# Performance work log

Hardware: AMD Instinct MI355X
Metric: run time of the kernel (lower is better)

Reference implementation:

```python
import jax, jax.numpy as jnp
import numpy as np

K = 3            # receptive_field
N = 50000        # num_nodes
E = 800000       # num_edges
D = 128          # feature dim


def setup_inputs() -> dict:
    key = jax.random.key(0)
    k1, k2, k3 = jax.random.split(key, 3)
    x = jax.random.normal(k1, (N, D), dtype=jnp.float32)
    edge_index = jax.random.randint(k2, (2, E), 0, N, dtype=jnp.int64)
    edge_weight = jax.random.uniform(k3, (E,), dtype=jnp.float32)
    return {"x": x, "edge_index": edge_index, "edge_weight": edge_weight}


def _gcn_norm(edge_weight, row, col, num_nodes):
    # symmetric GCN normalization: w_ij / sqrt(deg_i * deg_j), in-degree at target
    deg = jax.ops.segment_sum(edge_weight, col, num_segments=num_nodes)
    dinv = jnp.where(deg > 0, jax.lax.rsqrt(deg), 0.0)
    return dinv[row] * edge_weight * dinv[col]


def _propagate(x, row, col, w, num_nodes):
    # out[i] = sum_{(j->i) in E} w_ji * x[j]   (gather-scale-scatter)
    msgs = x[row] * w[:, None]                 # [E, D]
    return jax.ops.segment_sum(msgs, col, num_segments=num_nodes)


def reference(x, edge_index, edge_weight):
    num_nodes = x.shape[-2]
    row, col = edge_index[0], edge_index[1]
    w = _gcn_norm(edge_weight, row, col, num_nodes)
    out = [x]
    xk = x
    for _ in range(K):
        xk = _propagate(xk, row, col, w, num_nodes)
        out.append(xk)
    # global attribute: broadcast node-mean to every node
    g = jnp.broadcast_to(jnp.mean(x, axis=-2, keepdims=True), x.shape)
    out.append(g)
    return jnp.concatenate(out, axis=-1)   # [N, (K+2)*D]
```

## Files before the change

kernel.cpp:

```cpp
#include <hip/hip_runtime.h>


#define D 128
#define OUTC4 160
#define CAP 64
#define CH 8
#define PB 256
#define CB 512
#define BCAP 5120

__device__ inline unsigned short f2bf(float f) {
    unsigned u = __float_as_uint(f);
    u += 0x7FFFu + ((u >> 16) & 1u);
    return (unsigned short)(u >> 16);
}
__device__ inline float bfhi(unsigned u) {
    return __uint_as_float(u & 0xFFFF0000u);
}
__device__ inline float bflo(unsigned u) {
    return __uint_as_float(u << 16);
}
__device__ inline unsigned pack2(float lo, float hi) {
    return ((unsigned)f2bf(hi) << 16) | (unsigned)f2bf(lo);
}
__device__ inline void fma8(float4& a0, float4& a1, float w, uint4 v) {
    a0.x += w * bflo(v.x); a0.y += w * bfhi(v.x);
    a0.z += w * bflo(v.y); a0.w += w * bfhi(v.y);
    a1.x += w * bflo(v.z); a1.y += w * bfhi(v.z);
    a1.z += w * bflo(v.w); a1.w += w * bfhi(v.w);
}

__global__ void k_part(const int* __restrict__ row, const int* __restrict__ col,
                       const float* __restrict__ ew, const float* __restrict__ x,
                       int* __restrict__ bcur, uint2* __restrict__ breg,
                       float* __restrict__ gsum, int E, int N) {
    __shared__ int shi[512];
    if ((int)blockIdx.x < PB) {
        int* hist = shi;
        int* base = shi + 256;
        int rng = (E + PB - 1) / PB;
        int e0 = blockIdx.x * rng;
        int e1 = e0 + rng; if (e1 > E) e1 = E;
        hist[threadIdx.x] = 0;
        __syncthreads();
        for (int e = e0 + (int)threadIdx.x; e < e1; e += 256)
            atomicAdd(&hist[(unsigned)col[e] >> 8], 1);
        __syncthreads();
        int h = hist[threadIdx.x];
        if (h) base[threadIdx.x] = atomicAdd(&bcur[threadIdx.x], h);
        __syncthreads();
        hist[threadIdx.x] = 0;
        __syncthreads();
        for (int e = e0 + (int)threadIdx.x; e < e1; e += 256) {
            int c = col[e];
            int b = (unsigned)c >> 8;
            int r = atomicAdd(&hist[b], 1);
            int pos = base[b] + r;
            if (pos < BCAP)
                breg[(size_t)b * BCAP + pos] =
                    make_uint2(((unsigned)f2bf(ew[e]) << 16) | (unsigned)row[e], (unsigned)c);
        }
    } else {
        float* sh = (float*)shi;
        int bid = blockIdx.x - PB;
        int f = threadIdx.x & 127;
        int sub = threadIdx.x >> 7;
        float acc = 0.f;
        for (int n = bid * 2 + sub; n < N; n += CB * 2)
            acc += x[(size_t)n * D + f];
        if (sub) sh[f] = acc;
        __syncthreads();
        if (!sub) atomicAdd(&gsum[f], acc + sh[f]);
    }
}

__global__ void k_prep(const int* __restrict__ bcur, const uint2* __restrict__ breg,
                       int* __restrict__ cnt, float* __restrict__ dinv,
                       unsigned* __restrict__ slots, const float4* __restrict__ x4,
                       const float* __restrict__ gsum, float4* __restrict__ out4,
                       uint4* __restrict__ xb0, int N, int GB, float invN) {
    __shared__ int shi[512];
    if ((int)blockIdx.x < GB) {
        int* ncur = shi;
        float* wsum = (float*)(shi + 256);
        int b = blockIdx.x;
        ncur[threadIdx.x] = 0;
        wsum[threadIdx.x] = 0.f;
        __syncthreads();
        int cb = bcur[b]; if (cb > BCAP) cb = BCAP;
        const uint2* br = breg + (size_t)b * BCAP;
        for (int i = threadIdx.x; i < cb; i += 256) {
            uint2 ed = br[i];
            int node = (int)ed.y;
            int l = node & 255;
            int r = atomicAdd(&ncur[l], 1);
            if (r < CAP) slots[(size_t)node * CAP + r] = ed.x;
            atomicAdd(&wsum[l], bfhi(ed.x));
        }
        __syncthreads();
        int node = b * 256 + (int)threadIdx.x;
        if (node < N) {
            cnt[node] = ncur[threadIdx.x];
            float v = wsum[threadIdx.x];
            dinv[node] = v > 0.f ? rsqrtf(v) : 0.f;
        }
    } else {
        int t = (blockIdx.x - GB) * 256 + threadIdx.x;
        if (t >= N * 16) return;
        int n = t >> 4;
        int q = t & 15;
        float4 v0 = x4[(size_t)n * 32 + 2 * q];
        float4 v1 = x4[(size_t)n * 32 + 2 * q + 1];
        size_t ob = (size_t)n * OUTC4;
        out4[ob + 2 * q] = v0;
        out4[ob + 2 * q + 1] = v1;
        xb0[(size_t)n * 16 + q] = make_uint4(pack2(v0.x, v0.y), pack2(v0.z, v0.w),
                                             pack2(v1.x, v1.y), pack2(v1.z, v1.w));
        int g = 8 * q;
        out4[ob + 128 + 2 * q] = make_float4(gsum[g] * invN, gsum[g + 1] * invN,
                                             gsum[g + 2] * invN, gsum[g + 3] * invN);
        out4[ob + 129 + 2 * q] = make_float4(gsum[g + 4] * invN, gsum[g + 5] * invN,
                                             gsum[g + 6] * invN, gsum[g + 7] * invN);
    }
}

template <bool NORM>
__global__ void k_prop(const int* __restrict__ cnt, unsigned* __restrict__ slots,
                       const float* __restrict__ dinv, const uint4* __restrict__ xin,
                       float4* __restrict__ out4, uint4* __restrict__ xout,
                       int N, int out_off4, int writeb) {
    int t = blockIdx.x * blockDim.x + threadIdx.x;
    int node = t >> 4;
    if (node >= N) return;
    int lane = t & 15;
    int c = cnt[node]; if (c > CAP) c = CAP;
    unsigned* s = slots + (size_t)node * CAP;
    float dd = NORM ? dinv[node] : 0.f;
    float4 a0 = make_float4(0.f, 0.f, 0.f, 0.f);
    float4 a1 = make_float4(0.f, 0.f, 0.f, 0.f);
    int i = 0;
    for (; i + CH <= c; i += CH) {
        unsigned sl[CH]; float w[CH]; uint4 v[CH];
#pragma unroll
        for (int j = 0; j < CH; j++) sl[j] = s[i + j];
#pragma unroll
        for (int j = 0; j < CH; j++)
            w[j] = NORM ? dd * bfhi(sl[j]) * dinv[sl[j] & 0xFFFFu] : bfhi(sl[j]);
        if (NORM && lane == 0) {
#pragma unroll
            for (int j = 0; j < CH; j++)
                s[i + j] = ((unsigned)f2bf(w[j]) << 16) | (sl[j] & 0xFFFFu);
        }
#pragma unroll
        for (int j = 0; j < CH; j++) v[j] = xin[(size_t)(sl[j] & 0xFFFFu) * 16 + lane];
#pragma unroll
        for (int j = 0; j < CH; j++) fma8(a0, a1, w[j], v[j]);
    }
    if (i < c) {
        unsigned sl[CH]; float w[CH]; uint4 v[CH];
#pragma unroll
        for (int j = 0; j < CH; j++) {
            int idx = (i + j < c) ? i + j : c - 1;
            sl[j] = s[idx];
        }
#pragma unroll
        for (int j = 0; j < CH; j++) {
            float ww = NORM ? dd * bfhi(sl[j]) * dinv[sl[j] & 0xFFFFu] : bfhi(sl[j]);
            w[j] = (i + j < c) ? ww : 0.f;
        }
        if (NORM && lane == 0) {
#pragma unroll
            for (int j = 0; j < CH; j++)
                if (i + j < c) s[i + j] = ((unsigned)f2bf(w[j]) << 16) | (sl[j] & 0xFFFFu);
        }
#pragma unroll
        for (int j = 0; j < CH; j++) v[j] = xin[(size_t)(sl[j] & 0xFFFFu) * 16 + lane];
#pragma unroll
        for (int j = 0; j < CH; j++) fma8(a0, a1, w[j], v[j]);
    }
    size_t ob = (size_t)node * OUTC4 + out_off4 + 2 * lane;
    out4[ob] = a0;
    out4[ob + 1] = a1;
    if (writeb)
        xout[(size_t)node * 16 + lane] =
            make_uint4(pack2(a0.x, a0.y), pack2(a0.z, a0.w),
                       pack2(a1.x, a1.y), pack2(a1.z, a1.w));
}

extern "C" void kernel_launch(void* const* d_in, const int* in_sizes, int n_in,
                              void* d_out, int out_size, void* d_ws, size_t ws_size,
                              hipStream_t stream) {
    const float* x = (const float*)d_in[0];
    const int* ei = (const int*)d_in[1];
    const float* ew = (const float*)d_in[2];
    float* out = (float*)d_out;

    int N = in_sizes[0] / D;
    int E = in_sizes[2];
    const int* row = ei;
    const int* colp = ei + E;

    int* bcur = (int*)d_ws;
    float* gsum = (float*)(bcur + 256);
    int* cnt = (int*)(gsum + 128);
    float* dinv = (float*)(cnt + N);
    unsigned* slots = (unsigned*)(dinv + N);
    uint2* breg = (uint2*)(slots + (size_t)N * CAP);
    uint4* xb0 = (uint4*)(breg + (size_t)PB * BCAP);
    uint4* xb1 = xb0 + (size_t)N * 16;

    hipMemsetAsync(d_ws, 0, 384 * sizeof(int), stream);

    k_part<<<PB + CB, 256, 0, stream>>>(row, colp, ew, x, bcur, breg, gsum, E, N);

    int GB = (N + 255) / 256;
    int IB = (N * 16 + 255) / 256;
    k_prep<<<GB + IB, 256, 0, stream>>>(bcur, breg, cnt, dinv, slots, (const float4*)x,
                                        gsum, (float4*)out, xb0, N, GB, 1.f / (float)N);

    int pblocks = (N * 16 + 255) / 256;
    k_prop<true><<<pblocks, 256, 0, stream>>>(cnt, slots, dinv, xb0, (float4*)out, xb1, N, 32, 1);
    k_prop<false><<<pblocks, 256, 0, stream>>>(cnt, slots, dinv, xb1, (float4*)out, xb0, N, 64, 1);
    k_prop<false><<<pblocks, 256, 0, stream>>>(cnt, slots, dinv, xb0, (float4*)out, xb1, N, 96, 0);
}
```

Baseline: 283.2 us.

## Split later propagation hops into feature-slice passes and use nontemporal stores

```diff
diff --git a/kernel.cpp b/kernel.cpp
--- a/kernel.cpp
+++ b/kernel.cpp
@@ -8,6 +8,18 @@
 #define PB 256
 #define CB 512
 #define BCAP 5120
+
+typedef float f4v __attribute__((ext_vector_type(4)));
+typedef unsigned u4v __attribute__((ext_vector_type(4)));
+
+__device__ inline void nt_store_f4(float4* p, float4 v) {
+    f4v t = {v.x, v.y, v.z, v.w};
+    __builtin_nontemporal_store(t, (f4v*)p);
+}
+__device__ inline void nt_store_u4(uint4* p, uint4 v) {
+    u4v t = {v.x, v.y, v.z, v.w};
+    __builtin_nontemporal_store(t, (u4v*)p);
+}
 
 __device__ inline unsigned short f2bf(float f) {
     unsigned u = __float_as_uint(f);
@@ -112,30 +124,32 @@
         float4 v0 = x4[(size_t)n * 32 + 2 * q];
         float4 v1 = x4[(size_t)n * 32 + 2 * q + 1];
         size_t ob = (size_t)n * OUTC4;
-        out4[ob + 2 * q] = v0;
-        out4[ob + 2 * q + 1] = v1;
-        xb0[(size_t)n * 16 + q] = make_uint4(pack2(v0.x, v0.y), pack2(v0.z, v0.w),
-                                             pack2(v1.x, v1.y), pack2(v1.z, v1.w));
+        nt_store_f4(&out4[ob + 2 * q], v0);
+        nt_store_f4(&out4[ob + 2 * q + 1], v1);
+        nt_store_u4(&xb0[(size_t)n * 16 + q],
+                    make_uint4(pack2(v0.x, v0.y), pack2(v0.z, v0.w),
+                               pack2(v1.x, v1.y), pack2(v1.z, v1.w)));
         int g = 8 * q;
-        out4[ob + 128 + 2 * q] = make_float4(gsum[g] * invN, gsum[g + 1] * invN,
-                                             gsum[g + 2] * invN, gsum[g + 3] * invN);
-        out4[ob + 129 + 2 * q] = make_float4(gsum[g + 4] * invN, gsum[g + 5] * invN,
-                                             gsum[g + 6] * invN, gsum[g + 7] * invN);
-    }
-}
-
-template <bool NORM>
-__global__ void k_prop(const int* __restrict__ cnt, unsigned* __restrict__ slots,
-                       const float* __restrict__ dinv, const uint4* __restrict__ xin,
-                       float4* __restrict__ out4, uint4* __restrict__ xout,
-                       int N, int out_off4, int writeb) {
+        nt_store_f4(&out4[ob + 128 + 2 * q],
+                    make_float4(gsum[g] * invN, gsum[g + 1] * invN,
+                                gsum[g + 2] * invN, gsum[g + 3] * invN));
+        nt_store_f4(&out4[ob + 129 + 2 * q],
+                    make_float4(gsum[g + 4] * invN, gsum[g + 5] * invN,
+                                gsum[g + 6] * invN, gsum[g + 7] * invN));
+    }
+}
+
+__global__ void k_prop1(const int* __restrict__ cnt, unsigned* __restrict__ slots,
+                        const float* __restrict__ dinv, const uint4* __restrict__ xin,
+                        float4* __restrict__ out4, uint4* __restrict__ xout,
+                        int N, int out_off4) {
     int t = blockIdx.x * blockDim.x + threadIdx.x;
     int node = t >> 4;
     if (node >= N) return;
     int lane = t & 15;
     int c = cnt[node]; if (c > CAP) c = CAP;
     unsigned* s = slots + (size_t)node * CAP;
-    float dd = NORM ? dinv[node] : 0.f;
+    float dd = dinv[node];
     float4 a0 = make_float4(0.f, 0.f, 0.f, 0.f);
     float4 a1 = make_float4(0.f, 0.f, 0.f, 0.f);
     int i = 0;
@@ -145,8 +159,8 @@
         for (int j = 0; j < CH; j++) sl[j] = s[i + j];
 #pragma unroll
         for (int j = 0; j < CH; j++)
-            w[j] = NORM ? dd * bfhi(sl[j]) * dinv[sl[j] & 0xFFFFu] : bfhi(sl[j]);
-        if (NORM && lane == 0) {
+            w[j] = dd * bfhi(sl[j]) * dinv[sl[j] & 0xFFFFu];
+        if (lane == 0) {
 #pragma unroll
             for (int j = 0; j < CH; j++)
                 s[i + j] = ((unsigned)f2bf(w[j]) << 16) | (sl[j] & 0xFFFFu);
@@ -165,10 +179,10 @@
         }
 #pragma unroll
         for (int j = 0; j < CH; j++) {
-            float ww = NORM ? dd * bfhi(sl[j]) * dinv[sl[j] & 0xFFFFu] : bfhi(sl[j]);
+            float ww = dd * bfhi(sl[j]) * dinv[sl[j] & 0xFFFFu];
             w[j] = (i + j < c) ? ww : 0.f;
         }
-        if (NORM && lane == 0) {
+        if (lane == 0) {
 #pragma unroll
             for (int j = 0; j < CH; j++)
                 if (i + j < c) s[i + j] = ((unsigned)f2bf(w[j]) << 16) | (sl[j] & 0xFFFFu);
@@ -179,12 +193,57 @@
         for (int j = 0; j < CH; j++) fma8(a0, a1, w[j], v[j]);
     }
     size_t ob = (size_t)node * OUTC4 + out_off4 + 2 * lane;
-    out4[ob] = a0;
-    out4[ob + 1] = a1;
+    nt_store_f4(&out4[ob], a0);
+    nt_store_f4(&out4[ob + 1], a1);
+    nt_store_u4(&xout[(size_t)node * 16 + lane],
+                make_uint4(pack2(a0.x, a0.y), pack2(a0.z, a0.w),
+                           pack2(a1.x, a1.y), pack2(a1.z, a1.w)));
+}
+
+__global__ void k_pass(const int* __restrict__ cnt, const unsigned* __restrict__ slots,
+                       const uint4* __restrict__ xin, float4* __restrict__ out4,
+                       uint4* __restrict__ xout, int N, int out_off4, int pass,
+                       int writeb) {
+    int t = blockIdx.x * blockDim.x + threadIdx.x;
+    int node = t >> 2;
+    if (node >= N) return;
+    int lane = t & 3;
+    int c = cnt[node]; if (c > CAP) c = CAP;
+    const unsigned* s = slots + (size_t)node * CAP;
+    const uint4* xp = xin + 4 * pass + lane;
+    float4 a0 = make_float4(0.f, 0.f, 0.f, 0.f);
+    float4 a1 = make_float4(0.f, 0.f, 0.f, 0.f);
+    int i = 0;
+    for (; i + CH <= c; i += CH) {
+        unsigned sl[CH]; uint4 v[CH];
+#pragma unroll
+        for (int j = 0; j < CH; j++) sl[j] = __builtin_nontemporal_load(&s[i + j]);
+#pragma unroll
+        for (int j = 0; j < CH; j++) v[j] = xp[(size_t)(sl[j] & 0xFFFFu) * 16];
+#pragma unroll
+        for (int j = 0; j < CH; j++) fma8(a0, a1, bfhi(sl[j]), v[j]);
+    }
+    if (i < c) {
+        unsigned sl[CH]; float w[CH]; uint4 v[CH];
+#pragma unroll
+        for (int j = 0; j < CH; j++) {
+            int idx = (i + j < c) ? i + j : c - 1;
+            sl[j] = __builtin_nontemporal_load(&s[idx]);
+        }
+#pragma unroll
+        for (int j = 0; j < CH; j++) w[j] = (i + j < c) ? bfhi(sl[j]) : 0.f;
+#pragma unroll
+        for (int j = 0; j < CH; j++) v[j] = xp[(size_t)(sl[j] & 0xFFFFu) * 16];
+#pragma unroll
+        for (int j = 0; j < CH; j++) fma8(a0, a1, w[j], v[j]);
+    }
+    size_t ob = (size_t)node * OUTC4 + out_off4 + 8 * pass + 2 * lane;
+    nt_store_f4(&out4[ob], a0);
+    nt_store_f4(&out4[ob + 1], a1);
     if (writeb)
-        xout[(size_t)node * 16 + lane] =
-            make_uint4(pack2(a0.x, a0.y), pack2(a0.z, a0.w),
-                       pack2(a1.x, a1.y), pack2(a1.z, a1.w));
+        nt_store_u4(&xout[(size_t)node * 16 + 4 * pass + lane],
+                    make_uint4(pack2(a0.x, a0.y), pack2(a0.z, a0.w),
+                               pack2(a1.x, a1.y), pack2(a1.z, a1.w)));
 }
 
 extern "C" void kernel_launch(void* const* d_in, const int* in_sizes, int n_in,
@@ -219,7 +278,11 @@
                                         gsum, (float4*)out, xb0, N, GB, 1.f / (float)N);
 
     int pblocks = (N * 16 + 255) / 256;
-    k_prop<true><<<pblocks, 256, 0, stream>>>(cnt, slots, dinv, xb0, (float4*)out, xb1, N, 32, 1);
-    k_prop<false><<<pblocks, 256, 0, stream>>>(cnt, slots, dinv, xb1, (float4*)out, xb0, N, 64, 1);
-    k_prop<false><<<pblocks, 256, 0, stream>>>(cnt, slots, dinv, xb0, (float4*)out, xb1, N, 96, 0);
-}
+    k_prop1<<<pblocks, 256, 0, stream>>>(cnt, slots, dinv, xb0, (float4*)out, xb1, N, 32);
+
+    int qblocks = (N * 4 + 255) / 256;
+    for (int p = 0; p < 4; p++)
+        k_pass<<<qblocks, 256, 0, stream>>>(cnt, slots, xb1, (float4*)out, xb0, N, 64, p, 1);
+    for (int p = 0; p < 4; p++)
+        k_pass<<<qblocks, 256, 0, stream>>>(cnt, slots, xb0, (float4*)out, xb1, N, 96, p, 0);
+}
```

After: 401.4 us. 1.42x slower.

## Sort neighbor lists by source and sweep gathers in node-range phases

Applied to the files above, without the earlier changes.

```diff
diff --git a/kernel.cpp b/kernel.cpp
--- a/kernel.cpp
+++ b/kernel.cpp
@@ -4,10 +4,23 @@
 #define D 128
 #define OUTC4 160
 #define CAP 64
-#define CH 8
+#define CH 4
+#define NP 8
 #define PB 256
 #define CB 512
 #define BCAP 5120
+
+typedef float f4v __attribute__((ext_vector_type(4)));
+typedef unsigned u4v __attribute__((ext_vector_type(4)));
+
+__device__ inline void nt_store_f4(float4* p, float4 v) {
+    f4v t = {v.x, v.y, v.z, v.w};
+    __builtin_nontemporal_store(t, (f4v*)p);
+}
+__device__ inline void nt_store_u4(uint4* p, uint4 v) {
+    u4v t = {v.x, v.y, v.z, v.w};
+    __builtin_nontemporal_store(t, (u4v*)p);
+}
 
 __device__ inline unsigned short f2bf(float f) {
     unsigned u = __float_as_uint(f);
@@ -112,79 +125,103 @@
         float4 v0 = x4[(size_t)n * 32 + 2 * q];
         float4 v1 = x4[(size_t)n * 32 + 2 * q + 1];
         size_t ob = (size_t)n * OUTC4;
-        out4[ob + 2 * q] = v0;
-        out4[ob + 2 * q + 1] = v1;
+        nt_store_f4(&out4[ob + 2 * q], v0);
+        nt_store_f4(&out4[ob + 2 * q + 1], v1);
         xb0[(size_t)n * 16 + q] = make_uint4(pack2(v0.x, v0.y), pack2(v0.z, v0.w),
                                              pack2(v1.x, v1.y), pack2(v1.z, v1.w));
         int g = 8 * q;
-        out4[ob + 128 + 2 * q] = make_float4(gsum[g] * invN, gsum[g + 1] * invN,
-                                             gsum[g + 2] * invN, gsum[g + 3] * invN);
-        out4[ob + 129 + 2 * q] = make_float4(gsum[g + 4] * invN, gsum[g + 5] * invN,
-                                             gsum[g + 6] * invN, gsum[g + 7] * invN);
+        nt_store_f4(&out4[ob + 128 + 2 * q],
+                    make_float4(gsum[g] * invN, gsum[g + 1] * invN,
+                                gsum[g + 2] * invN, gsum[g + 3] * invN));
+        nt_store_f4(&out4[ob + 129 + 2 * q],
+                    make_float4(gsum[g + 4] * invN, gsum[g + 5] * invN,
+                                gsum[g + 6] * invN, gsum[g + 7] * invN));
     }
 }
 
 template <bool NORM>
-__global__ void k_prop(const int* __restrict__ cnt, unsigned* __restrict__ slots,
-                       const float* __restrict__ dinv, const uint4* __restrict__ xin,
-                       float4* __restrict__ out4, uint4* __restrict__ xout,
-                       int N, int out_off4, int writeb) {
-    int t = blockIdx.x * blockDim.x + threadIdx.x;
-    int node = t >> 4;
-    if (node >= N) return;
-    int lane = t & 15;
-    int c = cnt[node]; if (c > CAP) c = CAP;
-    unsigned* s = slots + (size_t)node * CAP;
-    float dd = NORM ? dinv[node] : 0.f;
+__global__ void k_hop(const int* __restrict__ cnt, unsigned* __restrict__ slots,
+                      const float* __restrict__ dinv, const uint4* __restrict__ xin,
+                      float4* __restrict__ out4, uint4* __restrict__ xout,
+                      int N, int out_off4, int writeb) {
+    __shared__ unsigned sls[16][65];
+    int nid = threadIdx.x >> 4;
+    int lane = threadIdx.x & 15;
+    int node = blockIdx.x * 16 + nid;
+    bool valid = node < N;
+    int c = 0;
+    unsigned* s = slots;
+    if (valid) {
+        c = cnt[node]; if (c > CAP) c = CAP;
+        s = slots + (size_t)node * CAP;
+        for (int i = lane; i < c; i += 16) sls[nid][i] = s[i];
+    }
+    __syncthreads();
+    if (NORM) {
+        unsigned vals[4]; int rks[4];
+#pragma unroll
+        for (int k = 0; k < 4; k++) {
+            int e = lane + 16 * k;
+            rks[k] = -1;
+            if (e < c) {
+                unsigned v = sls[nid][e];
+                unsigned key = v & 0xFFFFu;
+                int r = 0;
+                for (int f = 0; f < c; f++) {
+                    unsigned kf = sls[nid][f] & 0xFFFFu;
+                    r += (kf < key) || (kf == key && f < e);
+                }
+                vals[k] = v; rks[k] = r;
+            }
+        }
+        __syncthreads();
+#pragma unroll
+        for (int k = 0; k < 4; k++)
+            if (rks[k] >= 0) sls[nid][rks[k]] = vals[k];
+        __syncthreads();
+    }
+    float dd = (NORM && valid) ? dinv[node] : 0.f;
     float4 a0 = make_float4(0.f, 0.f, 0.f, 0.f);
     float4 a1 = make_float4(0.f, 0.f, 0.f, 0.f);
     int i = 0;
-    for (; i + CH <= c; i += CH) {
-        unsigned sl[CH]; float w[CH]; uint4 v[CH];
-#pragma unroll
-        for (int j = 0; j < CH; j++) sl[j] = s[i + j];
-#pragma unroll
-        for (int j = 0; j < CH; j++)
-            w[j] = NORM ? dd * bfhi(sl[j]) * dinv[sl[j] & 0xFFFFu] : bfhi(sl[j]);
-        if (NORM && lane == 0) {
+    for (int p = 1; p <= NP; p++) {
+        int lim = (int)(((long long)N * p) / NP);
+        int lo = i;
+        while (i < c && (int)(sls[nid][i] & 0xFFFFu) < lim) i++;
+        for (int q = lo; q < i; q += CH) {
+            unsigned sl[CH]; float w[CH]; uint4 v[CH];
+#pragma unroll
+            for (int j = 0; j < CH; j++) {
+                int idx = (q + j < i) ? q + j : i - 1;
+                sl[j] = sls[nid][idx];
+            }
+#pragma unroll
+            for (int j = 0; j < CH; j++) {
+                float ww = NORM ? dd * bfhi(sl[j]) * dinv[sl[j] & 0xFFFFu]
+                                : bfhi(sl[j]);
+                w[j] = (q + j < i) ? ww : 0.f;
+            }
+            if (NORM && lane == 0) {
+#pragma unroll
+                for (int j = 0; j < CH; j++)
+                    if (q + j < i)
+                        s[q + j] = ((unsigned)f2bf(w[j]) << 16) | (sl[j] & 0xFFFFu);
+            }
 #pragma unroll
             for (int j = 0; j < CH; j++)
-                s[i + j] = ((unsigned)f2bf(w[j]) << 16) | (sl[j] & 0xFFFFu);
-        }
-#pragma unroll
-        for (int j = 0; j < CH; j++) v[j] = xin[(size_t)(sl[j] & 0xFFFFu) * 16 + lane];
-#pragma unroll
-        for (int j = 0; j < CH; j++) fma8(a0, a1, w[j], v[j]);
-    }
-    if (i < c) {
-        unsigned sl[CH]; float w[CH]; uint4 v[CH];
-#pragma unroll
-        for (int j = 0; j < CH; j++) {
-            int idx = (i + j < c) ? i + j : c - 1;
-            sl[j] = s[idx];
-        }
-#pragma unroll
-        for (int j = 0; j < CH; j++) {
-            float ww = NORM ? dd * bfhi(sl[j]) * dinv[sl[j] & 0xFFFFu] : bfhi(sl[j]);
-            w[j] = (i + j < c) ? ww : 0.f;
-        }
-        if (NORM && lane == 0) {
-#pragma unroll
-            for (int j = 0; j < CH; j++)
-                if (i + j < c) s[i + j] = ((unsigned)f2bf(w[j]) << 16) | (sl[j] & 0xFFFFu);
-        }
-#pragma unroll
-        for (int j = 0; j < CH; j++) v[j] = xin[(size_t)(sl[j] & 0xFFFFu) * 16 + lane];
-#pragma unroll
-        for (int j = 0; j < CH; j++) fma8(a0, a1, w[j], v[j]);
-    }
+                v[j] = xin[(size_t)(sl[j] & 0xFFFFu) * 16 + lane];
+#pragma unroll
+            for (int j = 0; j < CH; j++) fma8(a0, a1, w[j], v[j]);
+        }
+    }
+    if (!valid) return;
     size_t ob = (size_t)node * OUTC4 + out_off4 + 2 * lane;
-    out4[ob] = a0;
-    out4[ob + 1] = a1;
+    nt_store_f4(&out4[ob], a0);
+    nt_store_f4(&out4[ob + 1], a1);
     if (writeb)
-        xout[(size_t)node * 16 + lane] =
-            make_uint4(pack2(a0.x, a0.y), pack2(a0.z, a0.w),
-                       pack2(a1.x, a1.y), pack2(a1.z, a1.w));
+        nt_store_u4(&xout[(size_t)node * 16 + lane],
+                    make_uint4(pack2(a0.x, a0.y), pack2(a0.z, a0.w),
+                               pack2(a1.x, a1.y), pack2(a1.z, a1.w)));
 }
 
 extern "C" void kernel_launch(void* const* d_in, const int* in_sizes, int n_in,
@@ -218,8 +255,8 @@
     k_prep<<<GB + IB, 256, 0, stream>>>(bcur, breg, cnt, dinv, slots, (const float4*)x,
                                         gsum, (float4*)out, xb0, N, GB, 1.f / (float)N);
 
-    int pblocks = (N * 16 + 255) / 256;
-    k_prop<true><<<pblocks, 256, 0, stream>>>(cnt, slots, dinv, xb0, (float4*)out, xb1, N, 32, 1);
-    k_prop<false><<<pblocks, 256, 0, stream>>>(cnt, slots, dinv, xb1, (float4*)out, xb0, N, 64, 1);
-    k_prop<false><<<pblocks, 256, 0, stream>>>(cnt, slots, dinv, xb0, (float4*)out, xb1, N, 96, 0);
-}
+    int hblocks = (N + 15) / 16;
+    k_hop<true><<<hblocks, 256, 0, stream>>>(cnt, slots, dinv, xb0, (float4*)out, xb1, N, 32, 1);
+    k_hop<false><<<hblocks, 256, 0, stream>>>(cnt, slots, dinv, xb1, (float4*)out, xb0, N, 64, 1);
+    k_hop<false><<<hblocks, 256, 0, stream>>>(cnt, slots, dinv, xb0, (float4*)out, xb1, N, 96, 0);
+}
```

After: 332.2 us. +17.3%, slower.
